# Kernel tuning notes

Hardware: AMD Instinct MI355X
Metric: run time of the kernel (lower is better)

## Reference

```python
import jax, jax.numpy as jnp
import numpy as np

B = 64          # graphs per batch
N_PER = 1024    # nodes per graph
N = B * N_PER   # 65536 total nodes
E_PER = 8192    # edges per graph (sorted by graph)
E = B * E_PER   # 524288 total edges
HID = 256       # config.model.dim_hidden
RATIO = 0.5     # causal_ratio
N_RES = int(RATIO * E_PER)  # edges kept per graph (n_reserve)


def setup_inputs() -> dict:
    key = jax.random.key(0)
    ks = jax.random.split(key, 12)
    x = jax.random.normal(ks[0], (N, HID), jnp.float32)
    # per-graph edges, no self-loops, sorted by graph id (split_batch assumption)
    base = jnp.repeat(jnp.arange(B, dtype=jnp.int32) * N_PER, E_PER)
    row_loc = jax.random.randint(ks[1], (E,), 0, N_PER, dtype=jnp.int32)
    off = jax.random.randint(ks[2], (E,), 1, N_PER, dtype=jnp.int32)
    col_loc = (row_loc + off) % N_PER
    edge_index = jnp.stack([base + row_loc, base + col_loc])  # [2, E]
    batch = jnp.repeat(jnp.arange(B, dtype=jnp.int32), N_PER)  # [N]

    def lin(k, fan_in, shape):
        return (jax.random.normal(k, shape, jnp.float32) / np.sqrt(fan_in)).astype(jnp.float32)

    # 2-layer GIN MLP params (eps = 0)
    W11 = lin(ks[3], HID, (HID, HID)); b11 = jnp.zeros((HID,), jnp.float32)
    W12 = lin(ks[4], HID, (HID, HID)); b12 = jnp.zeros((HID,), jnp.float32)
    W21 = lin(ks[5], HID, (HID, HID)); b21 = jnp.zeros((HID,), jnp.float32)
    W22 = lin(ks[6], HID, (HID, HID)); b22 = jnp.zeros((HID,), jnp.float32)
    # edge scoring linear: Linear(2*HID, 1)
    w_score = lin(ks[7], 2 * HID, (2 * HID,))
    b_score = jnp.zeros((), jnp.float32)
    return {"x": x, "edge_index": edge_index, "batch": batch,
            "W11": W11, "b11": b11, "W12": W12, "b12": b12,
            "W21": W21, "b21": b21, "W22": W22, "b22": b22,
            "w_score": w_score, "b_score": b_score}


def _gin_layer(h, row, col, W1, b1, W2, b2):
    agg = jax.ops.segment_sum(h[col], row, num_segments=N)  # sum over in-edges
    h = h + agg  # (1 + eps) * x + aggregate, eps = 0
    h = jax.nn.relu(h @ W1 + b1)
    return jax.nn.relu(h @ W2 + b2)


def _relabel(h, batch, ei_sub):
    # torch: sub_nodes = unique(edge_index); compact + remap. Padded to N for fixed shapes.
    sub = jnp.unique(ei_sub, size=N, fill_value=N)  # [N], padded with sentinel N
    node_idx = jnp.zeros((N + 1,), jnp.int32).at[sub].set(jnp.arange(N, dtype=jnp.int32))
    h_pad = jnp.concatenate([h, jnp.zeros((1, h.shape[1]), h.dtype)], axis=0)
    b_pad = jnp.concatenate([batch, jnp.full((1,), -1, batch.dtype)], axis=0)
    return h_pad[sub], node_idx[ei_sub], b_pad[sub]


def reference(x, edge_index, batch, W11, b11, W12, b12, W21, b21, W22, b22, w_score, b_score):
    row, col = edge_index[0], edge_index[1]
    h = _gin_layer(x, row, col, W11, b11, W12, b12)
    h = _gin_layer(h, row, col, W21, b21, W22, b22)  # [N, HID]

    # edge_score = Linear(cat(h[row], h[col])) without materializing [E, 2*HID]
    s_src = h @ w_score[:HID]   # [N]
    s_dst = h @ w_score[HID:]   # [N]
    edge_score = s_src[row] + s_dst[col] + b_score  # [E]

    # per-graph sort-based top-k split (split_graph), batched over B graphs
    s = edge_score.reshape(B, E_PER)
    rank = jnp.argsort(-s, axis=1)                      # descending
    idx_res, idx_drop = rank[:, :N_RES], rank[:, N_RES:]
    ei = edge_index.reshape(2, B, E_PER)

    def gather_edges(idx):
        return jnp.take_along_axis(ei, jnp.broadcast_to(idx[None], (2, B, idx.shape[1])), axis=2).reshape(2, -1)

    causal_ei = gather_edges(idx_res)
    conf_ei = gather_edges(idx_drop)
    causal_w = jnp.take_along_axis(s, idx_res, axis=1).reshape(-1)
    conf_w = -jnp.take_along_axis(s, idx_drop, axis=1).reshape(-1)

    causal_x, causal_ei_rel, causal_batch = _relabel(h, batch, causal_ei)
    conf_x, conf_ei_rel, conf_batch = _relabel(h, batch, conf_ei)

    return (causal_x, causal_ei_rel, causal_w, causal_batch,
            conf_x, conf_ei_rel, conf_w, conf_batch, edge_score)
```

## Files before the change

kernel.cpp:

```cpp
#include <hip/hip_runtime.h>
#include <hip/hip_bf16.h>

#define NN      65536
#define EE      524288
#define HIDC    256
#define BB      64
#define EPB     8192
#define NPB     1024
#define NRES    4096

#define O_CX    0
#define O_CEI   16777216
#define O_CW    17301504
#define O_CB    17563648
#define O_FX    17629184
#define O_FEI   34406400
#define O_FW    34930688
#define O_FB    35192832
#define O_ES    35258368

typedef __attribute__((ext_vector_type(8))) short short8v;
typedef __attribute__((ext_vector_type(4))) float f32x4;

__device__ __forceinline__ unsigned f2ord(float f) {
    unsigned u = __float_as_uint(f);
    return (u & 0x80000000u) ? ~u : (u | 0x80000000u);
}

__device__ __forceinline__ unsigned packsplit(float v) {
    unsigned u = __float_as_uint(v);
    unsigned hi = (u + 0x7FFFu + ((u >> 16) & 1u)) & 0xFFFF0000u;
    float lo = v - __uint_as_float(hi);
    unsigned ul = __float_as_uint(lo);
    unsigned lo16 = (ul + 0x7FFFu + ((ul >> 16) & 1u)) >> 16;
    return hi | lo16;
}

__global__ void k_init(int* __restrict__ flagC, int* __restrict__ flagF,
                       float* __restrict__ sSrc, float* __restrict__ sDst) {
    int v = blockIdx.x * blockDim.x + threadIdx.x;
    if (v < NN) { flagC[v] = 0; flagF[v] = 0; sSrc[v] = 0.f; sDst[v] = 0.f; }
}

__global__ void k_wsplit(const float* __restrict__ W11, const float* __restrict__ W12,
                         const float* __restrict__ W21, const float* __restrict__ W22,
                         unsigned* __restrict__ Wtp) {
    int g = blockIdx.x * 256 + threadIdx.x;
    int w = g >> 16, r = g & 65535;
    int n = r >> 8, k = r & 255;
    const float* W = (w == 0) ? W11 : (w == 1) ? W12 : (w == 2) ? W21 : W22;
    Wtp[g] = packsplit(W[k * 256 + n]);
}

__global__ __launch_bounds__(1024) void k_csr(const int* __restrict__ row,
                                              const int* __restrict__ col,
                                              int* __restrict__ rowPtr,
                                              int* __restrict__ colSorted) {
    __shared__ int hist[NPB];
    __shared__ int scn[NPB];
    int b = blockIdx.x, t = threadIdx.x;
    int base = b * EPB;
    hist[t] = 0;
    __syncthreads();
    int r[8], c[8];
#pragma unroll
    for (int j = 0; j < 8; ++j) {
        int e = base + t + j * 1024;
        r[j] = row[e] & (NPB - 1);
        c[j] = col[e];
        atomicAdd(&hist[r[j]], 1);
    }
    __syncthreads();
    int v = hist[t];
    scn[t] = v;
    __syncthreads();
    for (int off = 1; off < 1024; off <<= 1) {
        int a = (t >= off) ? scn[t - off] : 0;
        __syncthreads();
        scn[t] += a;
        __syncthreads();
    }
    int start = scn[t] - v;
    rowPtr[b * NPB + t] = base + start;
    if (b == 0 && t == 0) rowPtr[NN] = EE;
    hist[t] = start;
    __syncthreads();
#pragma unroll
    for (int j = 0; j < 8; ++j) {
        int pos = atomicAdd(&hist[r[j]], 1);
        colSorted[base + pos] = c[j];
    }
}

__global__ __launch_bounds__(256) void k_agg(const float* __restrict__ src,
                                             const float* __restrict__ resid,
                                             const int* __restrict__ colSorted,
                                             const int* __restrict__ rowPtr,
                                             unsigned* __restrict__ dstP) {
    int lane = threadIdx.x & 63;
    int v = blockIdx.x * 4 + (threadIdx.x >> 6);
    int e0 = rowPtr[v], e1 = rowPtr[v + 1];
    int cnt = e1 - e0;
    float4 acc = make_float4(0.f, 0.f, 0.f, 0.f);
    int myc = (lane < cnt) ? colSorted[e0 + lane] : 0;
    int lim = cnt < 64 ? cnt : 64;
    for (int base = 0; base < lim; base += 8) {
        int n = lim - base; if (n > 8) n = 8;
        float4 tv[8];
#pragma unroll
        for (int j = 0; j < 8; ++j)
            if (j < n) {
                int c = __shfl(myc, base + j, 64);
                tv[j] = *((const float4*)src + (size_t)c * 64 + lane);
            }
#pragma unroll
        for (int j = 0; j < 8; ++j)
            if (j < n) { acc.x += tv[j].x; acc.y += tv[j].y; acc.z += tv[j].z; acc.w += tv[j].w; }
    }
    for (int e = e0 + 64; e < e1; ++e) {
        int c = colSorted[e];
        float4 sv = *((const float4*)src + (size_t)c * 64 + lane);
        acc.x += sv.x; acc.y += sv.y; acc.z += sv.z; acc.w += sv.w;
    }
    float4 rv = *((const float4*)resid + (size_t)v * 64 + lane);
    uint4 o;
    o.x = packsplit(rv.x + acc.x);
    o.y = packsplit(rv.y + acc.y);
    o.z = packsplit(rv.z + acc.z);
    o.w = packsplit(rv.w + acc.w);
    *((uint4*)dstP + (size_t)v * 64 + lane) = o;
}

template<int EPI, int SC>
__global__ __launch_bounds__(256) void k_gemm_mfma(const unsigned* __restrict__ Ap,
                                                   const unsigned* __restrict__ Wtp,
                                                   const float* __restrict__ bias,
                                                   void* __restrict__ Cout,
                                                   const float* __restrict__ wsc,
                                                   float* __restrict__ sSrc,
                                                   float* __restrict__ sDst) {
    __shared__ short Ah[128][40];
    __shared__ short Al[128][40];
    __shared__ short Bh[128][40];
    __shared__ short Bl[128][40];
    int t = threadIdx.x;
    int lane = t & 63, wave = t >> 6;
    int bm = blockIdx.x * 128, bn = blockIdx.y * 128;
    int ln = lane & 15, qd = lane >> 4;
    f32x4 acc[2][8];
#pragma unroll
    for (int i = 0; i < 2; ++i)
#pragma unroll
        for (int j = 0; j < 8; ++j) acc[i][j] = (f32x4){0.f, 0.f, 0.f, 0.f};
    int row = t >> 1, half = t & 1;
    const uint4* ag = (const uint4*)(Ap + (size_t)(bm + row) * 256) + half * 4;
    const uint4* bg = (const uint4*)(Wtp + (size_t)(bn + row) * 256) + half * 4;
    for (int k0 = 0; k0 < 256; k0 += 32) {
        uint4 av[4], bv[4];
#pragma unroll
        for (int s = 0; s < 4; ++s) { av[s] = ag[s]; bv[s] = bg[s]; }
        ag += 8; bg += 8;
        __syncthreads();
#pragma unroll
        for (int s = 0; s < 4; ++s) {
            int kc = half * 16 + s * 4;
            *(short4*)&Ah[row][kc] = make_short4((short)(av[s].x >> 16), (short)(av[s].y >> 16),
                                                 (short)(av[s].z >> 16), (short)(av[s].w >> 16));
            *(short4*)&Al[row][kc] = make_short4((short)av[s].x, (short)av[s].y,
                                                 (short)av[s].z, (short)av[s].w);
            *(short4*)&Bh[row][kc] = make_short4((short)(bv[s].x >> 16), (short)(bv[s].y >> 16),
                                                 (short)(bv[s].z >> 16), (short)(bv[s].w >> 16));
            *(short4*)&Bl[row][kc] = make_short4((short)bv[s].x, (short)bv[s].y,
                                                 (short)bv[s].z, (short)bv[s].w);
        }
        __syncthreads();
        short8v ah0 = *(short8v*)&Ah[wave * 32 + ln][qd * 8];
        short8v ah1 = *(short8v*)&Ah[wave * 32 + 16 + ln][qd * 8];
        short8v al0 = *(short8v*)&Al[wave * 32 + ln][qd * 8];
        short8v al1 = *(short8v*)&Al[wave * 32 + 16 + ln][qd * 8];
#pragma unroll
        for (int nt = 0; nt < 8; ++nt) {
            short8v bh = *(short8v*)&Bh[nt * 16 + ln][qd * 8];
            short8v bl = *(short8v*)&Bl[nt * 16 + ln][qd * 8];
            f32x4 c0 = acc[0][nt];
            c0 = __builtin_amdgcn_mfma_f32_16x16x32_bf16(al0, bh, c0, 0, 0, 0);
            c0 = __builtin_amdgcn_mfma_f32_16x16x32_bf16(ah0, bl, c0, 0, 0, 0);
            c0 = __builtin_amdgcn_mfma_f32_16x16x32_bf16(ah0, bh, c0, 0, 0, 0);
            acc[0][nt] = c0;
            f32x4 c1 = acc[1][nt];
            c1 = __builtin_amdgcn_mfma_f32_16x16x32_bf16(al1, bh, c1, 0, 0, 0);
            c1 = __builtin_amdgcn_mfma_f32_16x16x32_bf16(ah1, bl, c1, 0, 0, 0);
            c1 = __builtin_amdgcn_mfma_f32_16x16x32_bf16(ah1, bh, c1, 0, 0, 0);
            acc[1][nt] = c1;
        }
    }
    float ps[2][4] = {}, pd[2][4] = {};
#pragma unroll
    for (int nt = 0; nt < 8; ++nt) {
        float bvs = bias[bn + nt * 16 + ln];
        float ws = 0.f, wd = 0.f;
        if (SC) { ws = wsc[bn + nt * 16 + ln]; wd = wsc[256 + bn + nt * 16 + ln]; }
#pragma unroll
        for (int mt = 0; mt < 2; ++mt)
#pragma unroll
            for (int r = 0; r < 4; ++r) {
                int gm = bm + wave * 32 + mt * 16 + qd * 4 + r;
                int gn = bn + nt * 16 + ln;
                float v = acc[mt][nt][r] + bvs;
                v = v > 0.f ? v : 0.f;
                if (SC) { ps[mt][r] += v * ws; pd[mt][r] += v * wd; }
                if (EPI == 0) ((unsigned*)Cout)[(size_t)gm * 256 + gn] = packsplit(v);
                else          ((float*)Cout)[(size_t)gm * 256 + gn] = v;
            }
    }
    if (SC) {
#pragma unroll
        for (int off = 1; off < 16; off <<= 1)
#pragma unroll
            for (int mt = 0; mt < 2; ++mt)
#pragma unroll
                for (int r = 0; r < 4; ++r) {
                    ps[mt][r] += __shfl_xor(ps[mt][r], off, 64);
                    pd[mt][r] += __shfl_xor(pd[mt][r], off, 64);
                }
        if (ln == 0) {
#pragma unroll
            for (int mt = 0; mt < 2; ++mt)
#pragma unroll
                for (int r = 0; r < 4; ++r) {
                    int gm = bm + wave * 32 + mt * 16 + qd * 4 + r;
                    atomicAdd(&sSrc[gm], ps[mt][r]);
                    atomicAdd(&sDst[gm], pd[mt][r]);
                }
        }
    }
}

__global__ void k_escore(const int* __restrict__ row, const int* __restrict__ col,
                         const float* __restrict__ sSrc, const float* __restrict__ sDst,
                         const float* __restrict__ bsc, float* __restrict__ out9) {
    int e = blockIdx.x * blockDim.x + threadIdx.x;
    if (e >= EE) return;
    out9[e] = sSrc[row[e]] + sDst[col[e]] + bsc[0];
}

__global__ __launch_bounds__(512) void k_sortS1(const float* __restrict__ esc,
                                                unsigned long long* __restrict__ keys) {
    __shared__ unsigned long long lds[4096];
    int blk = blockIdx.x, b = blk >> 1, c = blk & 1;
    int t = threadIdx.x;
    int gbase = b * EPB + c * 4096;
    for (int i = t; i < 4096; i += 512) {
        int idx = c * 4096 + i;
        unsigned m = f2ord(esc[b * EPB + idx]);
        lds[i] = ((unsigned long long)(~m) << 32) | (unsigned)idx;
    }
    __syncthreads();
    bool dirbit = (c != 0);
    for (int k = 2; k <= 4096; k <<= 1) {
        for (int j = k >> 1; j > 0; j >>= 1) {
            for (int t2 = t; t2 < 2048; t2 += 512) {
                int i = ((t2 & ~(j - 1)) << 1) | (t2 & (j - 1));
                int l = i | j;
                unsigned long long a = lds[i], d = lds[l];
                bool up = (((i & k) == 0) != dirbit);
                if ((a > d) == up) { lds[i] = d; lds[l] = a; }
            }
            __syncthreads();
        }
    }
    for (int i = t; i < 4096; i += 512) keys[gbase + i] = lds[i];
}

__global__ void k_sortS2(unsigned long long* __restrict__ keys) {
    int g = blockIdx.x * 256 + threadIdx.x;
    int b = g >> 12, i = g & 4095;
    unsigned long long* p = keys + b * EPB;
    unsigned long long a = p[i], d = p[i + 4096];
    if (a > d) { p[i] = d; p[i + 4096] = a; }
}

__global__ __launch_bounds__(512) void k_sortS3(const unsigned long long* __restrict__ keys,
                                                const int* __restrict__ row, const int* __restrict__ col,
                                                const float* __restrict__ esc,
                                                int* __restrict__ perm,
                                                int* __restrict__ flagC, int* __restrict__ flagF,
                                                float* __restrict__ outCW, float* __restrict__ outFW) {
    __shared__ unsigned long long lds[4096];
    int blk = blockIdx.x, b = blk >> 1, c = blk & 1;
    int gbase = b * EPB + c * 4096;
    int t = threadIdx.x;
    for (int i = t; i < 4096; i += 512) lds[i] = keys[gbase + i];
    __syncthreads();
    for (int j = 2048; j > 0; j >>= 1) {
        for (int t2 = t; t2 < 2048; t2 += 512) {
            int i = ((t2 & ~(j - 1)) << 1) | (t2 & (j - 1));
            int l = i | j;
            unsigned long long a = lds[i], d = lds[l];
            if (a > d) { lds[i] = d; lds[l] = a; }
        }
        __syncthreads();
    }
    for (int i = t; i < 4096; i += 512) {
        int idx = (int)(lds[i] & 0x1FFFull);
        int ge = b * EPB + idx;
        perm[gbase + i] = idx;
        int r = row[ge], cl = col[ge];
        float s = esc[ge];
        if (c == 0) { flagC[r] = 1; flagC[cl] = 1; outCW[b * NRES + i] = s; }
        else        { flagF[r] = 1; flagF[cl] = 1; outFW[b * NRES + i] = -s; }
    }
}

__global__ __launch_bounds__(256) void k_scan1(const int* __restrict__ fc, const int* __restrict__ ff,
                                               int* __restrict__ bsC, int* __restrict__ bsF) {
    __shared__ int s1[256], s2[256];
    int t = threadIdx.x, v = blockIdx.x * 256 + t;
    s1[t] = fc[v]; s2[t] = ff[v];
    __syncthreads();
    for (int off = 128; off > 0; off >>= 1) {
        if (t < off) { s1[t] += s1[t + off]; s2[t] += s2[t + off]; }
        __syncthreads();
    }
    if (t == 0) { bsC[blockIdx.x] = s1[0]; bsF[blockIdx.x] = s2[0]; }
}

__global__ __launch_bounds__(256) void k_scan2(const int* __restrict__ bsC, const int* __restrict__ bsF,
                                               int* __restrict__ boC, int* __restrict__ boF,
                                               int* __restrict__ prefC, int* __restrict__ prefF) {
    __shared__ int s1[256], s2[256];
    int t = threadIdx.x;
    int v1 = bsC[t], v2 = bsF[t];
    s1[t] = v1; s2[t] = v2;
    __syncthreads();
    for (int off = 1; off < 256; off <<= 1) {
        int a1 = (t >= off) ? s1[t - off] : 0;
        int a2 = (t >= off) ? s2[t - off] : 0;
        __syncthreads();
        s1[t] += a1; s2[t] += a2;
        __syncthreads();
    }
    boC[t] = s1[t] - v1; boF[t] = s2[t] - v2;
    if (t == 255) { prefC[NN] = s1[255]; prefF[NN] = s2[255]; }
}

__global__ __launch_bounds__(256) void k_scan3(const int* __restrict__ fc, const int* __restrict__ ff,
                                               const int* __restrict__ boC, const int* __restrict__ boF,
                                               int* __restrict__ prefC, int* __restrict__ prefF) {
    __shared__ int s1[256], s2[256];
    int t = threadIdx.x, v = blockIdx.x * 256 + t;
    int f1 = fc[v], f2 = ff[v];
    s1[t] = f1; s2[t] = f2;
    __syncthreads();
    for (int off = 1; off < 256; off <<= 1) {
        int a1 = (t >= off) ? s1[t - off] : 0;
        int a2 = (t >= off) ? s2[t - off] : 0;
        __syncthreads();
        s1[t] += a1; s2[t] += a2;
        __syncthreads();
    }
    prefC[v] = boC[blockIdx.x] + s1[t] - f1;
    prefF[v] = boF[blockIdx.x] + s2[t] - f2;
}

__global__ __launch_bounds__(256) void k_scatter2(const int* __restrict__ flagC, const int* __restrict__ prefC,
                                                  const int* __restrict__ flagF, const int* __restrict__ prefF,
                                                  const float* __restrict__ h,
                                                  float* __restrict__ outCX, float* __restrict__ outCB,
                                                  float* __restrict__ outFX, float* __restrict__ outFB) {
    int lane = threadIdx.x & 63;
    int i = blockIdx.x * 4 + (threadIdx.x >> 6);
    int c0 = lane << 2;
    int fC = flagC[i], fF = flagF[i];
    float4 hv = make_float4(0.f, 0.f, 0.f, 0.f);
    if (fC | fF) hv = *(const float4*)(h + (size_t)i * HIDC + c0);
    if (fC) {
        int p = prefC[i];
        *(float4*)(outCX + (size_t)p * HIDC + c0) = hv;
        if (lane == 0) outCB[p] = (float)(i >> 10);
    }
    if (fF) {
        int p = prefF[i];
        *(float4*)(outFX + (size_t)p * HIDC + c0) = hv;
        if (lane == 0) outFB[p] = (float)(i >> 10);
    }
    int nuC = prefC[NN], nuF = prefF[NN];
    float4 z = make_float4(0.f, 0.f, 0.f, 0.f);
    if (i >= nuC) { *(float4*)(outCX + (size_t)i * HIDC + c0) = z; if (lane == 0) outCB[i] = -1.0f; }
    if (i >= nuF) { *(float4*)(outFX + (size_t)i * HIDC + c0) = z; if (lane == 0) outFB[i] = -1.0f; }
}

__global__ void k_eirel(const int* __restrict__ perm, const int* __restrict__ row,
                        const int* __restrict__ col, const int* __restrict__ prefC,
                        const int* __restrict__ prefF,
                        float* __restrict__ outC, float* __restrict__ outF) {
    int g = blockIdx.x * blockDim.x + threadIdx.x;
    if (g >= EE) return;
    int b = g >> 13, jj = g & (EPB - 1);
    int ge = (b << 13) | perm[g];
    int r = row[ge], c = col[ge];
    if (jj < NRES) {
        int idx = b * NRES + jj;
        outC[idx] = (float)prefC[r];
        outC[BB * NRES + idx] = (float)prefC[c];
    } else {
        int idx = b * NRES + (jj - NRES);
        outF[idx] = (float)prefF[r];
        outF[BB * NRES + idx] = (float)prefF[c];
    }
}

extern "C" void kernel_launch(void* const* d_in, const int* in_sizes, int n_in,
                              void* d_out, int out_size, void* d_ws, size_t ws_size,
                              hipStream_t stream) {
    const float* x   = (const float*)d_in[0];
    const int*   ei  = (const int*)d_in[1];
    const int*   row = ei;
    const int*   col = ei + EE;
    const float* W11 = (const float*)d_in[3];
    const float* b11 = (const float*)d_in[4];
    const float* W12 = (const float*)d_in[5];
    const float* b12 = (const float*)d_in[6];
    const float* W21 = (const float*)d_in[7];
    const float* b21 = (const float*)d_in[8];
    const float* W22 = (const float*)d_in[9];
    const float* b22 = (const float*)d_in[10];
    const float* wsc = (const float*)d_in[11];
    const float* bsc = (const float*)d_in[12];

    float* out = (float*)d_out;

    void* X = (void*)(out + O_CX);

    char* w = (char*)d_ws;
    auto alloc = [&](size_t bytes) { char* p = w; w += (bytes + 255) & ~(size_t)255; return p; };
    void*  P         = (void*)alloc((size_t)NN * HIDC * 4);
    float* sSrc      = (float*)alloc((size_t)NN * 4);
    float* sDst      = (float*)alloc((size_t)NN * 4);
    int*   colSorted = (int*)alloc((size_t)EE * 4);
    int*   rowPtr    = (int*)alloc((size_t)(NN + 1) * 4);
    int*   perm      = (int*)alloc((size_t)EE * 4);
    unsigned long long* keys64 = (unsigned long long*)alloc((size_t)EE * 8);
    int*   flagC     = (int*)alloc((size_t)NN * 4);
    int*   flagF     = (int*)alloc((size_t)NN * 4);
    int*   prefC     = (int*)alloc((size_t)(NN + 1) * 4);
    int*   prefF     = (int*)alloc((size_t)(NN + 1) * 4);
    unsigned* Wtp    = (unsigned*)alloc((size_t)4 * 65536 * 4);
    int*   bsC       = (int*)alloc(256 * 4);
    int*   bsF       = (int*)alloc(256 * 4);
    int*   boC       = (int*)alloc(256 * 4);
    int*   boF       = (int*)alloc(256 * 4);

    float* esc = out + O_ES;

    hipLaunchKernelGGL(k_init, dim3(NN / 256), dim3(256), 0, stream, flagC, flagF, sSrc, sDst);
    hipLaunchKernelGGL(k_wsplit, dim3(1024), dim3(256), 0, stream, W11, W12, W21, W22, Wtp);
    hipLaunchKernelGGL(k_csr, dim3(BB), dim3(1024), 0, stream, row, col, rowPtr, colSorted);

    dim3 ggrid(NN / 128, 2), gblk(256);

    hipLaunchKernelGGL(k_agg, dim3(NN / 4), dim3(256), 0, stream, x, x, colSorted, rowPtr, (unsigned*)X);
    k_gemm_mfma<0, 0><<<ggrid, gblk, 0, stream>>>((const unsigned*)X, Wtp + 0 * 65536, b11, P,
                                                  nullptr, nullptr, nullptr);
    k_gemm_mfma<1, 0><<<ggrid, gblk, 0, stream>>>((const unsigned*)P, Wtp + 1 * 65536, b12, X,
                                                  nullptr, nullptr, nullptr);
    hipLaunchKernelGGL(k_agg, dim3(NN / 4), dim3(256), 0, stream, (const float*)X, (const float*)X,
                       colSorted, rowPtr, (unsigned*)P);
    k_gemm_mfma<0, 0><<<ggrid, gblk, 0, stream>>>((const unsigned*)P, Wtp + 2 * 65536, b21, X,
                                                  nullptr, nullptr, nullptr);
    k_gemm_mfma<1, 1><<<ggrid, gblk, 0, stream>>>((const unsigned*)X, Wtp + 3 * 65536, b22, P,
                                                  wsc, sSrc, sDst);

    const float* h = (const float*)P;

    hipLaunchKernelGGL(k_escore, dim3(EE / 256), dim3(256), 0, stream, row, col, sSrc, sDst, bsc, esc);

    hipLaunchKernelGGL(k_sortS1, dim3(BB * 2), dim3(512), 0, stream, esc, keys64);
    hipLaunchKernelGGL(k_sortS2, dim3(EE / 512), dim3(256), 0, stream, keys64);
    hipLaunchKernelGGL(k_sortS3, dim3(BB * 2), dim3(512), 0, stream, keys64, row, col, esc,
                       perm, flagC, flagF, out + O_CW, out + O_FW);

    hipLaunchKernelGGL(k_scan1, dim3(NN / 256), dim3(256), 0, stream, flagC, flagF, bsC, bsF);
    hipLaunchKernelGGL(k_scan2, dim3(1), dim3(256), 0, stream, bsC, bsF, boC, boF, prefC, prefF);
    hipLaunchKernelGGL(k_scan3, dim3(NN / 256), dim3(256), 0, stream, flagC, flagF, boC, boF, prefC, prefF);

    hipLaunchKernelGGL(k_scatter2, dim3(NN / 4), dim3(256), 0, stream, flagC, prefC, flagF, prefF, h,
                       out + O_CX, out + O_CB, out + O_FX, out + O_FB);
    hipLaunchKernelGGL(k_eirel, dim3(EE / 256), dim3(256), 0, stream, perm, row, col,
                       prefC, prefF, out + O_CEI, out + O_FEI);
}
```

Measured before the change: 622.7 us.

## Stage per-graph feature slices in LDS for aggregation and fuse edge scoring into sort

Neighbour aggregation now gives each block one graph and one 16-float feature slice. The block loads all 1024 nodes of that slice into shared memory and gathers neighbours from LDS instead of making random global float4 loads. This relies on edges staying within a graph (col masked to the local node id). Edge scoring is folded into the first sort stage, which removes a kernel launch. The final sort stage rebuilds the score from the sort key instead of reading esc again. The new aggregation loop runs edge by edge per node with only 8 lanes per node, so it may lose memory-level parallelism and suffer load imbalance.

```diff
diff --git a/kernel.cpp b/kernel.cpp
--- a/kernel.cpp
+++ b/kernel.cpp
@@ -26,6 +26,10 @@
     unsigned u = __float_as_uint(f);
     return (u & 0x80000000u) ? ~u : (u | 0x80000000u);
 }
+__device__ __forceinline__ float ord2f(unsigned m) {
+    unsigned u = (m & 0x80000000u) ? (m & 0x7FFFFFFFu) : ~m;
+    return __uint_as_float(u);
+}
 
 __device__ __forceinline__ unsigned packsplit(float v) {
     unsigned u = __float_as_uint(v);
@@ -92,43 +96,38 @@
     }
 }
 
-__global__ __launch_bounds__(256) void k_agg(const float* __restrict__ src,
-                                             const float* __restrict__ resid,
-                                             const int* __restrict__ colSorted,
-                                             const int* __restrict__ rowPtr,
-                                             unsigned* __restrict__ dstP) {
-    int lane = threadIdx.x & 63;
-    int v = blockIdx.x * 4 + (threadIdx.x >> 6);
-    int e0 = rowPtr[v], e1 = rowPtr[v + 1];
-    int cnt = e1 - e0;
-    float4 acc = make_float4(0.f, 0.f, 0.f, 0.f);
-    int myc = (lane < cnt) ? colSorted[e0 + lane] : 0;
-    int lim = cnt < 64 ? cnt : 64;
-    for (int base = 0; base < lim; base += 8) {
-        int n = lim - base; if (n > 8) n = 8;
-        float4 tv[8];
-#pragma unroll
-        for (int j = 0; j < 8; ++j)
-            if (j < n) {
-                int c = __shfl(myc, base + j, 64);
-                tv[j] = *((const float4*)src + (size_t)c * 64 + lane);
-            }
-#pragma unroll
-        for (int j = 0; j < 8; ++j)
-            if (j < n) { acc.x += tv[j].x; acc.y += tv[j].y; acc.z += tv[j].z; acc.w += tv[j].w; }
-    }
-    for (int e = e0 + 64; e < e1; ++e) {
-        int c = colSorted[e];
-        float4 sv = *((const float4*)src + (size_t)c * 64 + lane);
-        acc.x += sv.x; acc.y += sv.y; acc.z += sv.z; acc.w += sv.w;
-    }
-    float4 rv = *((const float4*)resid + (size_t)v * 64 + lane);
-    uint4 o;
-    o.x = packsplit(rv.x + acc.x);
-    o.y = packsplit(rv.y + acc.y);
-    o.z = packsplit(rv.z + acc.z);
-    o.w = packsplit(rv.w + acc.w);
-    *((uint4*)dstP + (size_t)v * 64 + lane) = o;
+__global__ __launch_bounds__(512) void k_agg_lds(const float* __restrict__ src,
+                                                 const int* __restrict__ colSorted,
+                                                 const int* __restrict__ rowPtr,
+                                                 unsigned* __restrict__ dstP) {
+    __shared__ float lds[NPB * 16];
+    int ch = blockIdx.x, b = blockIdx.y;
+    int t = threadIdx.x;
+    int nbase = b * NPB;
+    const float4* sp = (const float4*)src;
+    float4* lp4 = (float4*)lds;
+#pragma unroll
+    for (int p = 0; p < 8; ++p) {
+        int i = t + p * 512;
+        int node = i >> 2, f4 = i & 3;
+        lp4[node * 4 + f4] = sp[(size_t)(nbase + node) * 64 + ch * 4 + f4];
+    }
+    __syncthreads();
+    const float2* lds2 = (const float2*)lds;
+    int g = t >> 3, l = t & 7;
+    int v0 = nbase + g * 16;
+    for (int i = 0; i < 16; ++i) {
+        int v = v0 + i;
+        int e0 = rowPtr[v], e1 = rowPtr[v + 1];
+        float2 acc = lds2[(v - nbase) * 8 + l];
+        for (int e = e0; e < e1; ++e) {
+            int c = colSorted[e] & (NPB - 1);
+            float2 s = lds2[c * 8 + l];
+            acc.x += s.x; acc.y += s.y;
+        }
+        uint2 o = make_uint2(packsplit(acc.x), packsplit(acc.y));
+        *((uint2*)dstP + (size_t)v * 128 + ch * 8 + l) = o;
+    }
 }
 
 template<int EPI, int SC>
@@ -236,23 +235,22 @@
     }
 }
 
-__global__ void k_escore(const int* __restrict__ row, const int* __restrict__ col,
-                         const float* __restrict__ sSrc, const float* __restrict__ sDst,
-                         const float* __restrict__ bsc, float* __restrict__ out9) {
-    int e = blockIdx.x * blockDim.x + threadIdx.x;
-    if (e >= EE) return;
-    out9[e] = sSrc[row[e]] + sDst[col[e]] + bsc[0];
-}
-
-__global__ __launch_bounds__(512) void k_sortS1(const float* __restrict__ esc,
+__global__ __launch_bounds__(512) void k_sortS1(const int* __restrict__ row, const int* __restrict__ col,
+                                                const float* __restrict__ sSrc, const float* __restrict__ sDst,
+                                                const float* __restrict__ bsc,
+                                                float* __restrict__ esc,
                                                 unsigned long long* __restrict__ keys) {
     __shared__ unsigned long long lds[4096];
     int blk = blockIdx.x, b = blk >> 1, c = blk & 1;
     int t = threadIdx.x;
     int gbase = b * EPB + c * 4096;
+    float bb = bsc[0];
     for (int i = t; i < 4096; i += 512) {
         int idx = c * 4096 + i;
-        unsigned m = f2ord(esc[b * EPB + idx]);
+        int ge = b * EPB + idx;
+        float s = sSrc[row[ge]] + sDst[col[ge]] + bb;
+        esc[ge] = s;
+        unsigned m = f2ord(s);
         lds[i] = ((unsigned long long)(~m) << 32) | (unsigned)idx;
     }
     __syncthreads();
@@ -282,7 +280,6 @@
 
 __global__ __launch_bounds__(512) void k_sortS3(const unsigned long long* __restrict__ keys,
                                                 const int* __restrict__ row, const int* __restrict__ col,
-                                                const float* __restrict__ esc,
                                                 int* __restrict__ perm,
                                                 int* __restrict__ flagC, int* __restrict__ flagF,
                                                 float* __restrict__ outCW, float* __restrict__ outFW) {
@@ -302,11 +299,12 @@
         __syncthreads();
     }
     for (int i = t; i < 4096; i += 512) {
-        int idx = (int)(lds[i] & 0x1FFFull);
+        unsigned long long kk = lds[i];
+        int idx = (int)(kk & 0x1FFFull);
         int ge = b * EPB + idx;
         perm[gbase + i] = idx;
         int r = row[ge], cl = col[ge];
-        float s = esc[ge];
+        float s = ord2f(~(unsigned)(kk >> 32));
         if (c == 0) { flagC[r] = 1; flagC[cl] = 1; outCW[b * NRES + i] = s; }
         else        { flagF[r] = 1; flagF[cl] = 1; outFW[b * NRES + i] = -s; }
     }
@@ -458,14 +456,15 @@
     hipLaunchKernelGGL(k_csr, dim3(BB), dim3(1024), 0, stream, row, col, rowPtr, colSorted);
 
     dim3 ggrid(NN / 128, 2), gblk(256);
-
-    hipLaunchKernelGGL(k_agg, dim3(NN / 4), dim3(256), 0, stream, x, x, colSorted, rowPtr, (unsigned*)X);
+    dim3 agrid(16, BB), ablk(512);
+
+    hipLaunchKernelGGL(k_agg_lds, agrid, ablk, 0, stream, x, colSorted, rowPtr, (unsigned*)X);
     k_gemm_mfma<0, 0><<<ggrid, gblk, 0, stream>>>((const unsigned*)X, Wtp + 0 * 65536, b11, P,
                                                   nullptr, nullptr, nullptr);
     k_gemm_mfma<1, 0><<<ggrid, gblk, 0, stream>>>((const unsigned*)P, Wtp + 1 * 65536, b12, X,
                                                   nullptr, nullptr, nullptr);
-    hipLaunchKernelGGL(k_agg, dim3(NN / 4), dim3(256), 0, stream, (const float*)X, (const float*)X,
-                       colSorted, rowPtr, (unsigned*)P);
+    hipLaunchKernelGGL(k_agg_lds, agrid, ablk, 0, stream, (const float*)X, colSorted, rowPtr,
+                       (unsigned*)P);
     k_gemm_mfma<0, 0><<<ggrid, gblk, 0, stream>>>((const unsigned*)P, Wtp + 2 * 65536, b21, X,
                                                   nullptr, nullptr, nullptr);
     k_gemm_mfma<1, 1><<<ggrid, gblk, 0, stream>>>((const unsigned*)X, Wtp + 3 * 65536, b22, P,
@@ -473,11 +472,10 @@
 
     const float* h = (const float*)P;
 
-    hipLaunchKernelGGL(k_escore, dim3(EE / 256), dim3(256), 0, stream, row, col, sSrc, sDst, bsc, esc);
-
-    hipLaunchKernelGGL(k_sortS1, dim3(BB * 2), dim3(512), 0, stream, esc, keys64);
+    hipLaunchKernelGGL(k_sortS1, dim3(BB * 2), dim3(512), 0, stream, row, col, sSrc, sDst, bsc,
+                       esc, keys64);
     hipLaunchKernelGGL(k_sortS2, dim3(EE / 512), dim3(256), 0, stream, keys64);
-    hipLaunchKernelGGL(k_sortS3, dim3(BB * 2), dim3(512), 0, stream, keys64, row, col, esc,
+    hipLaunchKernelGGL(k_sortS3, dim3(BB * 2), dim3(512), 0, stream, keys64, row, col,
                        perm, flagC, flagF, out + O_CW, out + O_FW);
 
     hipLaunchKernelGGL(k_scan1, dim3(NN / 256), dim3(256), 0, stream, flagC, flagF, bsC, bsF);
```

Measured after the change: 706.7 us. 1.13x slower.
